# Optimization experiments

Measured on AMD Instinct MI355X. Metric: run time of the kernel, lower is better.

The kernel has to match this reference:

```python
import jax, jax.numpy as jnp
import numpy as np

H = 8          # num query heads
KV = 1         # num kv heads
D = 256        # head_dim
HID = 2048     # hidden_size
B = 4          # sequences in prefill batch
S = 2048       # tokens per sequence
T = B * S      # total tokens
NUM_SLOTS = 16384
ROPE_THETA = 10000.0


def setup_inputs() -> dict:
    key = jax.random.key(0)
    k1, k2, k3 = jax.random.split(key, 3)
    hidden_states = jax.random.normal(k1, (T, HID), dtype=jnp.float32)
    # real rotary tables: positions 0..S-1 repeated per sequence
    pos = jnp.tile(jnp.arange(S, dtype=jnp.float32), B)              # [T]
    inv_freq = 1.0 / (ROPE_THETA ** (jnp.arange(0, D, 2, dtype=jnp.float32) / D))  # [D/2]
    ang = pos[:, None] * inv_freq[None, :]                            # [T, D/2]
    cos, sin = jnp.cos(ang), jnp.sin(ang)
    slots = jnp.arange(T, dtype=jnp.int32)                            # contiguous slot mapping
    key_cache = jnp.zeros((NUM_SLOTS, KV, D), dtype=jnp.float32)
    value_cache = jnp.zeros((NUM_SLOTS, KV, D), dtype=jnp.float32)
    w_qkv = jax.random.normal(k2, ((H + 2 * KV) * D, HID), dtype=jnp.float32) * (HID ** -0.5)
    w_o = jax.random.normal(k3, (HID, H * D), dtype=jnp.float32) * ((H * D) ** -0.5)
    return {"hidden_states": hidden_states, "cos": cos, "sin": sin, "slots": slots,
            "key_cache": key_cache, "value_cache": value_cache, "w_qkv": w_qkv, "w_o": w_o}


def _rope(x, cos, sin):
    # rotate-half convention: x:[T, h, D], cos/sin:[T, D/2]
    x1, x2 = x[..., : D // 2], x[..., D // 2 :]
    c, s = cos[:, None, :], sin[:, None, :]
    return jnp.concatenate([x1 * c - x2 * s, x2 * c + x1 * s], axis=-1)


def reference(hidden_states, cos, sin, slots, key_cache, value_cache, w_qkv, w_o):
    qkv = hidden_states @ w_qkv.T                                  # [T, (H+2KV)*D]
    q = qkv[:, : H * D].reshape(T, H, D)
    k = qkv[:, H * D : (H + KV) * D].reshape(T, KV, D)
    v = qkv[:, (H + KV) * D :].reshape(T, KV, D)
    q = _rope(q, cos, sin)
    k = _rope(k, cos, sin)
    # paged_attention.reshape_and_cache: scatter post-RoPE k and raw v into cache slots
    key_cache = key_cache.at[slots].set(k)
    value_cache = value_cache.at[slots].set(v)
    # prefill flash attention: causal, per-sequence (equal-length ragged batch)
    qb = q.reshape(B, S, H, D)
    kb = jnp.repeat(k.reshape(B, S, KV, D), H // KV, axis=2)       # GQA expand
    vb = jnp.repeat(v.reshape(B, S, KV, D), H // KV, axis=2)
    scale = D ** -0.5
    scores = jnp.einsum("bqhd,bkhd->bhqk", qb, kb) * scale          # [B,H,S,S]
    causal = jnp.tril(jnp.ones((S, S), dtype=bool))
    scores = jnp.where(causal[None, None], scores, jnp.finfo(scores.dtype).min)
    probs = jax.nn.softmax(scores, axis=-1)
    attn = jnp.einsum("bhqk,bkhd->bqhd", probs, vb).reshape(T, H * D)
    out = attn @ w_o.T                                              # [T, HID]
    return out, key_cache, value_cache
```

## Files before the change

kernel.cpp:

```cpp
#include <hip/hip_runtime.h>

#define HN 8
#define DH 256
#define HID 2048
#define BB 4
#define SS 2048
#define TT (BB*SS)
#define NQKV 2560
#define NSLOTS 16384

typedef unsigned short u16;
typedef unsigned int u32;
typedef __bf16 bf16x8 __attribute__((ext_vector_type(8)));
typedef float f32x4 __attribute__((ext_vector_type(4)));
typedef u16 u16x4 __attribute__((ext_vector_type(4)));
typedef u16 u16x8 __attribute__((ext_vector_type(8)));

__device__ __forceinline__ u16 f2bf(float f) {
    u32 u = __builtin_bit_cast(u32, f);
    u = u + 0x7fffu + ((u >> 16) & 1u);
    return (u16)(u >> 16);
}
__device__ __forceinline__ float bf2f(u16 h) {
    u32 u = ((u32)h) << 16;
    return __builtin_bit_cast(float, u);
}
__device__ __forceinline__ void gload_lds16(const void* g, void* l) {
    __builtin_amdgcn_global_load_lds((__attribute__((address_space(1))) void*)g,
                                     (__attribute__((address_space(3))) void*)l,
                                     16, 0, 0);
}
__device__ __forceinline__ u32 cvtpk_bf16(float a, float b) {
    u32 r;
    asm("v_cvt_pk_bf16_f32 %0, %1, %2" : "=v"(r) : "v"(a), "v"(b));
    return r;
}

__global__ __launch_bounds__(256) void cvt_f32_bf16(const float* __restrict__ in,
                                                    u16* __restrict__ out, long n) {
    long i = ((long)blockIdx.x * blockDim.x + threadIdx.x) * 4;
    long stride = (long)gridDim.x * blockDim.x * 4;
    for (; i < n; i += stride) {
        float4 v = *(const float4*)(in + i);
        u16x4 o4;
        o4[0] = f2bf(v.x); o4[1] = f2bf(v.y); o4[2] = f2bf(v.z); o4[3] = f2bf(v.w);
        *(u16x4*)(out + i) = o4;
    }
}

template<int OUTBF>
__global__ __launch_bounds__(256) void gemm_nt(const u16* __restrict__ A, const u16* __restrict__ B,
                                               void* __restrict__ C, int M, int N, int K) {
    __shared__ u16 As[128 * 32];
    __shared__ u16 Bs[128 * 32];
    const int tid = threadIdx.x;
    const int lane = tid & 63, w = tid >> 6;
    const int quad = lane >> 4, m16 = lane & 15;
    const int wm = w & 1, wn = w >> 1;
    const int r4 = tid >> 2, c8 = (tid & 3) * 8;
    const long arow = (long)blockIdx.x * 128;
    const long brow = (long)blockIdx.y * 128;

    f32x4 acc[4][4];
#pragma unroll
    for (int i = 0; i < 4; i++)
#pragma unroll
        for (int j = 0; j < 4; j++) acc[i][j] = (f32x4){0.f, 0.f, 0.f, 0.f};

    const u16* Ag = A + (arow + r4) * (long)K + c8;
    const u16* Bg = B + (brow + r4) * (long)K + c8;

    for (int k0 = 0; k0 < K; k0 += 32) {
        __syncthreads();
        gload_lds16(Ag + k0,                 (char*)As + tid * 16);
        gload_lds16(Ag + 64l * K + k0,       (char*)As + 4096 + tid * 16);
        gload_lds16(Bg + k0,                 (char*)Bs + tid * 16);
        gload_lds16(Bg + 64l * K + k0,       (char*)Bs + 4096 + tid * 16);
        __syncthreads();
        bf16x8 af[4], bfr[4];
#pragma unroll
        for (int mi = 0; mi < 4; mi++)
            af[mi] = *(const bf16x8*)(As + (wm * 64 + mi * 16 + m16) * 32 + quad * 8);
#pragma unroll
        for (int ni = 0; ni < 4; ni++)
            bfr[ni] = *(const bf16x8*)(Bs + (wn * 64 + ni * 16 + m16) * 32 + quad * 8);
#pragma unroll
        for (int mi = 0; mi < 4; mi++)
#pragma unroll
            for (int ni = 0; ni < 4; ni++)
                acc[mi][ni] = __builtin_amdgcn_mfma_f32_16x16x32_bf16(af[mi], bfr[ni], acc[mi][ni], 0, 0, 0);
    }
#pragma unroll
    for (int mi = 0; mi < 4; mi++) {
#pragma unroll
        for (int ni = 0; ni < 4; ni++) {
            long col = brow + wn * 64 + ni * 16 + m16;
#pragma unroll
            for (int r = 0; r < 4; r++) {
                long row = arow + wm * 64 + mi * 16 + quad * 4 + r;
                float v = acc[mi][ni][r];
                if (OUTBF) ((u16*)C)[row * N + col] = f2bf(v);
                else       ((float*)C)[row * N + col] = v;
            }
        }
    }
}

__global__ __launch_bounds__(256) void rope_scatter(u16* __restrict__ qkv, const float* __restrict__ cosb,
        const float* __restrict__ sinb, const int* __restrict__ slots,
        u16* __restrict__ kb, float* __restrict__ kc, float* __restrict__ vc) {
    const int t = blockIdx.x, tid = threadIdx.x;
    const long qbase = (long)t * NQKV;
#pragma unroll
    for (int i = 0; i < 4; i++) {
        int idx = tid + i * 256;
        int head = idx >> 7, d = idx & 127;
        long off = qbase + head * DH + d;
        float q1 = bf2f(qkv[off]), q2 = bf2f(qkv[off + 128]);
        float c = cosb[(long)t * 128 + d], s = sinb[(long)t * 128 + d];
        qkv[off]       = f2bf((q1 * c - q2 * s) * 0.0625f);
        qkv[off + 128] = f2bf((q2 * c + q1 * s) * 0.0625f);
    }
    const int slot = slots[t];
    if (tid < 128) {
        int d = tid;
        long off = qbase + HN * DH + d;
        float k1 = bf2f(qkv[off]), k2 = bf2f(qkv[off + 128]);
        float c = cosb[(long)t * 128 + d], s = sinb[(long)t * 128 + d];
        float kn1 = k1 * c - k2 * s, kn2 = k2 * c + k1 * s;
        kb[(long)t * DH + d]       = f2bf(kn1);
        kb[(long)t * DH + d + 128] = f2bf(kn2);
        kc[(long)slot * DH + d]       = kn1;
        kc[(long)slot * DH + d + 128] = kn2;
    }
    {
        int d = tid;
        vc[(long)slot * DH + d] = bf2f(qkv[qbase + (HN + 1) * DH + d]);
    }
}

__global__ __launch_bounds__(256) void transpose_v(const u16* __restrict__ qkv, u16* __restrict__ vbt) {
    const int tid = threadIdx.x;
    const int s0 = blockIdx.x * 64, d0 = blockIdx.y * 64, b = blockIdx.z;
#pragma unroll
    for (int i = 0; i < 2; i++) {
        int d = d0 + i * 32 + (tid >> 3);
        int s = s0 + (tid & 7) * 8;
        u16x8 v;
#pragma unroll
        for (int e = 0; e < 8; e++)
            v[e] = qkv[(long)(b * SS + s + e) * NQKV + (HN + 1) * DH + d];
        *(u16x8*)(vbt + ((long)b * DH + d) * SS + s) = v;
    }
}

__global__ __launch_bounds__(256, 4) void flash_attn(const u16* __restrict__ qkv, const u16* __restrict__ kb,
                                                     const u16* __restrict__ vbt, u16* __restrict__ attn) {
    __shared__ u16 Ks[32 * 256];
    __shared__ u16 Vt[256 * 32];
    const int tid = threadIdx.x;
    const int lane = tid & 63, w = tid >> 6;
    const int quad = lane >> 4, m16 = lane & 15;
    const int xr = blockIdx.x & 7, xt = blockIdx.x >> 3;
    const int qb = (xt == 0) ? 31 - xr : (xt == 1) ? 16 + xr : (xt == 2) ? 15 - xr : xr;
    const int h = blockIdx.y, b = blockIdx.z;
    const int qrow_w = qb * 64 + w * 16;

    const int krow = tid >> 5, kg = tid & 31, kgs = kg ^ krow;
    const int ks_hi = (krow >> 2) << 3, ks_lo = krow & 3;
    const int vrow = tid >> 2, vg = tid & 3,  vgs = vg ^ ((vrow >> 1) & 3);
    const int km7 = m16 & 7;
    const int vcol = (quad ^ ((m16 >> 1) & 3)) * 8;

    bf16x8 aq[8];
    {
        const u16* qp = qkv + (long)(b * SS + qrow_w + m16) * NQKV + h * DH;
#pragma unroll
        for (int ks = 0; ks < 8; ks++)
            aq[ks] = *(const bf16x8*)(qp + ks * 32 + quad * 8);
    }
    f32x4 o[16];
#pragma unroll
    for (int i = 0; i < 16; i++) o[i] = (f32x4){0.f, 0.f, 0.f, 0.f};
    float m_run = -1e30f;
    float l_run = 0.f;
    const long kvrow0 = (long)b * SS;
    const u16* vbase = vbt + (long)b * DH * SS;
    const int ntiles = 2 * qb + 2;

    for (int it = 0; it < ntiles; it++) {
        const int kv0 = it * 32;
        __syncthreads();
#pragma unroll
        for (int i = 0; i < 4; i++) {
            const int srcrow = ((i & 1) << 4) + ks_hi + ((i >> 1) << 2) + ks_lo;
            gload_lds16(kb + (kvrow0 + kv0 + srcrow) * DH + kgs * 8,
                        (char*)Ks + i * 4096 + tid * 16);
            gload_lds16(vbase + (long)(i * 64 + vrow) * SS + kv0 + vgs * 8,
                        (char*)Vt + i * 4096 + tid * 16);
        }
        asm volatile("s_waitcnt vmcnt(0)" ::: "memory");
        __syncthreads();

        if (kv0 <= qrow_w + 15) {
            f32x4 sc[2];
            sc[0] = (f32x4){0.f, 0.f, 0.f, 0.f};
            sc[1] = (f32x4){0.f, 0.f, 0.f, 0.f};
            __builtin_amdgcn_s_setprio(1);
#pragma unroll
            for (int ks = 0; ks < 8; ks++)
#pragma unroll
                for (int n = 0; n < 2; n++) {
                    bf16x8 kf = *(const bf16x8*)(Ks + (n * 16 + m16) * 256 + (((ks * 4 + quad) ^ km7) << 3));
                    sc[n] = __builtin_amdgcn_mfma_f32_16x16x32_bf16(kf, aq[ks], sc[n], 0, 0, 0);
                }
            __builtin_amdgcn_s_setprio(0);
            if (kv0 >= qb * 64) {
                const int qg = qrow_w + m16;
                const int kvb = kv0 + quad * 8;
#pragma unroll
                for (int n = 0; n < 2; n++)
#pragma unroll
                    for (int r = 0; r < 4; r++)
                        if (kvb + n * 4 + r > qg) sc[n][r] = -1e30f;
            }
            float mx = fmaxf(fmaxf(fmaxf(sc[0][0], sc[0][1]), fmaxf(sc[0][2], sc[0][3])),
                             fmaxf(fmaxf(sc[1][0], sc[1][1]), fmaxf(sc[1][2], sc[1][3])));
            if (__any((int)(mx > m_run + 8.f))) {
                float mr = fmaxf(mx, __shfl_xor(mx, 16));
                mr = fmaxf(mr, __shfl_xor(mr, 32));
                float mn = fmaxf(m_run, mr);
                float alpha = __expf(m_run - mn);
                m_run = mn;
                l_run *= alpha;
                float ar[4];
#pragma unroll
                for (int r = 0; r < 4; r++) ar[r] = __shfl(alpha, quad * 4 + r);
#pragma unroll
                for (int nf = 0; nf < 16; nf++)
#pragma unroll
                    for (int r = 0; r < 4; r++) o[nf][r] *= ar[r];
            }
#pragma unroll
            for (int n = 0; n < 2; n++)
#pragma unroll
                for (int r = 0; r < 4; r++) {
                    float p = __expf(sc[n][r] - m_run);
                    sc[n][r] = p;
                    l_run += p;
                }
            union { u32 w4[4]; bf16x8 v; } pu;
            pu.w4[0] = cvtpk_bf16(sc[0][0], sc[0][1]);
            pu.w4[1] = cvtpk_bf16(sc[0][2], sc[0][3]);
            pu.w4[2] = cvtpk_bf16(sc[1][0], sc[1][1]);
            pu.w4[3] = cvtpk_bf16(sc[1][2], sc[1][3]);
            __builtin_amdgcn_s_setprio(1);
#pragma unroll
            for (int nf = 0; nf < 16; nf++) {
                bf16x8 vf = *(const bf16x8*)(Vt + (nf * 16 + m16) * 32 + vcol);
                o[nf] = __builtin_amdgcn_mfma_f32_16x16x32_bf16(pu.v, vf, o[nf], 0, 0, 0);
            }
            __builtin_amdgcn_s_setprio(0);
        }
    }
    l_run += __shfl_xor(l_run, 16);
    l_run += __shfl_xor(l_run, 32);
    float invm = 1.f / l_run;
    float ir[4];
#pragma unroll
    for (int r = 0; r < 4; r++) ir[r] = __shfl(invm, quad * 4 + r);
#pragma unroll
    for (int nf = 0; nf < 16; nf++)
#pragma unroll
        for (int r = 0; r < 4; r++) {
            long row = (long)(b * SS + qrow_w + quad * 4 + r);
            attn[row * (HN * DH) + h * DH + nf * 16 + m16] = f2bf(o[nf][r] * ir[r]);
        }
}

extern "C" void kernel_launch(void* const* d_in, const int* in_sizes, int n_in,
                              void* d_out, int out_size, void* d_ws, size_t ws_size,
                              hipStream_t stream) {
    (void)in_sizes; (void)n_in; (void)out_size; (void)ws_size;
    const float* hidden = (const float*)d_in[0];
    const float* cosb   = (const float*)d_in[1];
    const float* sinb   = (const float*)d_in[2];
    const int*   slots  = (const int*)d_in[3];
    const float* kc_in  = (const float*)d_in[4];
    const float* vc_in  = (const float*)d_in[5];
    const float* w_qkv  = (const float*)d_in[6];
    const float* w_o    = (const float*)d_in[7];

    float* out    = (float*)d_out;
    float* kc_out = out + (size_t)TT * HID;
    float* vc_out = kc_out + (size_t)NSLOTS * DH;

    char* p = (char*)d_ws;
    u16* hid_b  = (u16*)p;  p += (size_t)TT * HID * 2;
    u16* wqkv_b = (u16*)p;  p += (size_t)NQKV * HID * 2;
    u16* wo_b   = (u16*)p;  p += (size_t)HID * HID * 2;
    u16* kb     = (u16*)p;  p += (size_t)TT * DH * 2;
    u16* vbt    = (u16*)p;  p += (size_t)TT * DH * 2;
    u16* attn_b = hid_b;
    u16* qkv_b  = (u16*)d_out;

    hipMemcpyAsync(kc_out, kc_in, (size_t)NSLOTS * DH * 4, hipMemcpyDeviceToDevice, stream);
    hipMemcpyAsync(vc_out, vc_in, (size_t)NSLOTS * DH * 4, hipMemcpyDeviceToDevice, stream);

    cvt_f32_bf16<<<dim3(2048), dim3(256), 0, stream>>>(hidden, hid_b, (long)TT * HID);
    cvt_f32_bf16<<<dim3(640),  dim3(256), 0, stream>>>(w_qkv, wqkv_b, (long)NQKV * HID);
    cvt_f32_bf16<<<dim3(512),  dim3(256), 0, stream>>>(w_o,   wo_b,   (long)HID * HID);

    gemm_nt<1><<<dim3(TT / 128, NQKV / 128), dim3(256), 0, stream>>>(hid_b, wqkv_b, qkv_b, TT, NQKV, HID);
    rope_scatter<<<dim3(TT), dim3(256), 0, stream>>>(qkv_b, cosb, sinb, slots, kb, kc_out, vc_out);
    transpose_v<<<dim3(SS / 64, DH / 64, BB), dim3(256), 0, stream>>>(qkv_b, vbt);
    flash_attn<<<dim3(SS / 64, HN, BB), dim3(256), 0, stream>>>(qkv_b, kb, vbt, attn_b);
    gemm_nt<0><<<dim3(TT / 128, HID / 128), dim3(256), 0, stream>>>(attn_b, wo_b, out, TT, HID, HID);
}
```

Baseline: 646.4 us.

## Prefetch KV tiles into registers, swizzle GEMM blocks, tile V transpose via LDS

The flash-attention loop now loads the next K/V tile into registers while the current tile is computed, then writes those registers to LDS at the start of the next iteration. This replaces the synchronous direct-to-LDS loads that waited on vmcnt(0) each iteration. The GEMM kernel remaps block indices with a grouped swizzle to improve L2 reuse. The V transpose now stages 64x64 tiles through padded shared memory so both the global reads and the writes are coalesced. The register prefetch adds VGPR pressure to a kernel launched with occupancy 4.

```diff
diff --git a/kernel.cpp b/kernel.cpp
--- a/kernel.cpp
+++ b/kernel.cpp
@@ -58,8 +58,11 @@
     const int quad = lane >> 4, m16 = lane & 15;
     const int wm = w & 1, wn = w >> 1;
     const int r4 = tid >> 2, c8 = (tid & 3) * 8;
-    const long arow = (long)blockIdx.x * 128;
-    const long brow = (long)blockIdx.y * 128;
+    const int nwg = gridDim.x * gridDim.y;
+    const int lin = blockIdx.x + gridDim.x * blockIdx.y;
+    const int swz = (lin & 7) * (nwg >> 3) + (lin >> 3);
+    const long arow = (long)(swz % gridDim.x) * 128;
+    const long brow = (long)(swz / gridDim.x) * 128;
 
     f32x4 acc[4][4];
 #pragma unroll
@@ -140,17 +143,24 @@
 }
 
 __global__ __launch_bounds__(256) void transpose_v(const u16* __restrict__ qkv, u16* __restrict__ vbt) {
+    __shared__ u16 Ls[64][66];
     const int tid = threadIdx.x;
     const int s0 = blockIdx.x * 64, d0 = blockIdx.y * 64, b = blockIdx.z;
+    const int lr = tid >> 3, lc = (tid & 7) * 8;
 #pragma unroll
     for (int i = 0; i < 2; i++) {
-        int d = d0 + i * 32 + (tid >> 3);
-        int s = s0 + (tid & 7) * 8;
+        int s = s0 + i * 32 + lr;
+        u16x8 v = *(const u16x8*)(qkv + (long)(b * SS + s) * NQKV + (HN + 1) * DH + d0 + lc);
+        *(u16x8*)(&Ls[i * 32 + lr][lc]) = v;
+    }
+    __syncthreads();
+#pragma unroll
+    for (int i = 0; i < 2; i++) {
+        int d = i * 32 + lr;
         u16x8 v;
 #pragma unroll
-        for (int e = 0; e < 8; e++)
-            v[e] = qkv[(long)(b * SS + s + e) * NQKV + (HN + 1) * DH + d];
-        *(u16x8*)(vbt + ((long)b * DH + d) * SS + s) = v;
+        for (int e = 0; e < 8; e++) v[e] = Ls[lc + e][d];
+        *(u16x8*)(vbt + ((long)b * DH + d0 + d) * SS + s0 + lc) = v;
     }
 }
 
@@ -188,19 +198,34 @@
     const u16* vbase = vbt + (long)b * DH * SS;
     const int ntiles = 2 * qb + 2;
 
+    u16x8 kreg[4], vreg[4];
+    {
+#pragma unroll
+        for (int i = 0; i < 4; i++) {
+            const int srcrow = ((i & 1) << 4) + ks_hi + ((i >> 1) << 2) + ks_lo;
+            kreg[i] = *(const u16x8*)(kb + (kvrow0 + srcrow) * DH + kgs * 8);
+            vreg[i] = *(const u16x8*)(vbase + (long)(i * 64 + vrow) * SS + vgs * 8);
+        }
+    }
+
     for (int it = 0; it < ntiles; it++) {
         const int kv0 = it * 32;
         __syncthreads();
 #pragma unroll
         for (int i = 0; i < 4; i++) {
-            const int srcrow = ((i & 1) << 4) + ks_hi + ((i >> 1) << 2) + ks_lo;
-            gload_lds16(kb + (kvrow0 + kv0 + srcrow) * DH + kgs * 8,
-                        (char*)Ks + i * 4096 + tid * 16);
-            gload_lds16(vbase + (long)(i * 64 + vrow) * SS + kv0 + vgs * 8,
-                        (char*)Vt + i * 4096 + tid * 16);
-        }
-        asm volatile("s_waitcnt vmcnt(0)" ::: "memory");
+            *(u16x8*)((char*)Ks + i * 4096 + tid * 16) = kreg[i];
+            *(u16x8*)((char*)Vt + i * 4096 + tid * 16) = vreg[i];
+        }
         __syncthreads();
+        if (it + 1 < ntiles) {
+            const int kv1 = kv0 + 32;
+#pragma unroll
+            for (int i = 0; i < 4; i++) {
+                const int srcrow = ((i & 1) << 4) + ks_hi + ((i >> 1) << 2) + ks_lo;
+                kreg[i] = *(const u16x8*)(kb + (kvrow0 + kv1 + srcrow) * DH + kgs * 8);
+                vreg[i] = *(const u16x8*)(vbase + (long)(i * 64 + vrow) * SS + kv1 + vgs * 8);
+            }
+        }
 
         if (kv0 <= qrow_w + 15) {
             f32x4 sc[2];
```

Result: slower. 882.5 us (+36.5%).
